# Kernel tuning notes

Measured on AMD Instinct MI355X. Metric: run time of the kernel, lower is better.

Reference implementation:

```python
import jax, jax.numpy as jnp
import numpy as np

B, L, D, H = 2, 2048, 1024, 16
NUM_BUCKETS, MAX_DISTANCE = 32, 128


def _rel_pos_buckets(qlen, klen, num_buckets, max_distance):
    """T5-style bidirectional relative position bucketing. Returns [qlen, klen] int32."""
    ctx = jnp.arange(qlen, dtype=jnp.int32)[:, None]
    mem = jnp.arange(klen, dtype=jnp.int32)[None, :]
    rel = mem - ctx  # memory_position - context_position
    nb = num_buckets // 2
    buckets = (rel > 0).astype(jnp.int32) * nb
    n = jnp.abs(rel)
    max_exact = nb // 2
    is_small = n < max_exact
    nf = jnp.maximum(n.astype(jnp.float32), 1.0)
    large = max_exact + (
        jnp.log(nf / max_exact) / np.float32(np.log(max_distance / max_exact)) * (nb - max_exact)
    ).astype(jnp.int32)
    large = jnp.minimum(large, nb - 1)
    return buckets + jnp.where(is_small, n, large)


def setup_inputs() -> dict:
    key = jax.random.key(0)
    ks = jax.random.split(key, 11)
    s = 0.02
    return {
        "x": jax.random.normal(ks[0], (B, L, D), dtype=jnp.float32),
        "mask": jax.random.randint(ks[1], (B, 1, L, L), 0, 2, dtype=jnp.int32),
        "Wq_w": jax.random.normal(ks[2], (D, D), dtype=jnp.float32) * s,
        "Wq_b": jnp.zeros((D,), dtype=jnp.float32),
        "Wk_w": jax.random.normal(ks[3], (D, D), dtype=jnp.float32) * s,
        "Wk_b": jnp.zeros((D,), dtype=jnp.float32),
        "Wv_w": jax.random.normal(ks[4], (D, D), dtype=jnp.float32) * s,
        "Wv_b": jnp.zeros((D,), dtype=jnp.float32),
        "Wo_w": jax.random.normal(ks[5], (D, D), dtype=jnp.float32) * s,
        "Wo_b": jnp.zeros((D,), dtype=jnp.float32),
        "rel_emb": jax.random.normal(ks[6], (NUM_BUCKETS, H), dtype=jnp.float32) * s,
    }


def reference(x, mask, Wq_w, Wq_b, Wk_w, Wk_b, Wv_w, Wv_b, Wo_w, Wo_b, rel_emb):
    b, l, d = x.shape
    h = H
    dk = d // h
    # torch Linear: y = x @ W.T + b
    Q = (x @ Wq_w.T + Wq_b).reshape(b, l, h, dk)
    K = (x @ Wk_w.T + Wk_b).reshape(b, l, h, dk)
    V = (x @ Wv_w.T + Wv_b).reshape(b, l, h, dk)
    scores = jnp.einsum("bqhd,bkhd->bhqk", Q, K) / jnp.sqrt(jnp.float32(dk))
    buckets = _rel_pos_buckets(l, l, NUM_BUCKETS, MAX_DISTANCE)  # [L, L]
    bias = rel_emb[buckets]  # [L, L, H]
    scores = scores + jnp.transpose(bias, (2, 0, 1))[None]  # [1, H, L, L]
    scores = jnp.where(mask == 0, jnp.float32(-1e9), scores)
    attn = jax.nn.softmax(scores, axis=-1)
    out = jnp.einsum("bhqk,bkhd->bqhd", attn, V).reshape(b, l, d)
    return out @ Wo_w.T + Wo_b
```

## Files before the change

### kernel.cpp

```cpp
#include <hip/hip_runtime.h>
#include <hip/hip_fp16.h>

#define B_ 2
#define L_ 2048
#define D_ 1024
#define H_ 16

typedef __attribute__((ext_vector_type(8))) _Float16 f16x8;
typedef __attribute__((ext_vector_type(4))) _Float16 f16x4;
typedef __attribute__((ext_vector_type(2))) __fp16 fp16x2;
typedef __attribute__((ext_vector_type(4))) float f32x4;

#define LOG2E 1.44269504088896f

__device__ __forceinline__ void gload_lds16(const void* g, void* l) {
  __builtin_amdgcn_global_load_lds(
      (const __attribute__((address_space(1))) unsigned int*)g,
      (__attribute__((address_space(3))) unsigned int*)l, 16, 0, 0);
}

__global__ __launch_bounds__(256) void cvt_all(
    const float* __restrict__ x, const float* __restrict__ Wq,
    const float* __restrict__ Wk, const float* __restrict__ Wv,
    const float* __restrict__ Wo, __half* __restrict__ xh,
    __half* __restrict__ wqh, __half* __restrict__ wkh,
    __half* __restrict__ wvh, __half* __restrict__ woh) {
  int i = blockIdx.x * 256 + threadIdx.x;
  const float* src;
  __half* dst;
  int j;
  if (i < 1048576) {
    src = x; dst = xh; j = i;
  } else {
    int k = i - 1048576;
    int wsel = k >> 18;
    j = k & 262143;
    src = wsel == 0 ? Wq : (wsel == 1 ? Wk : (wsel == 2 ? Wv : Wo));
    dst = wsel == 0 ? wqh : (wsel == 1 ? wkh : (wsel == 2 ? wvh : woh));
  }
  float4 v = ((const float4*)src)[j];
  __half2* o = (__half2*)(dst + (size_t)j * 4);
  o[0] = __floats2half2_rn(v.x, v.y);
  o[1] = __floats2half2_rn(v.z, v.w);
}

__global__ __launch_bounds__(256) void pack_mask(const int* __restrict__ m,
                                                 unsigned long long* __restrict__ bits) {
  int wword = blockIdx.x * 4 + (threadIdx.x >> 6);
  int lane = threadIdx.x & 63;
  int v = m[(size_t)wword * 64 + lane];
  unsigned long long bal = __ballot(v != 0);
  if (lane == 0) bits[wword] = bal;
}

__global__ __launch_bounds__(256) void bias_table(const float* __restrict__ rel_emb,
                                                  float* __restrict__ tab) {
  int i = blockIdx.x * 256 + threadIdx.x;
  if (i >= H_ * 4095) return;
  int h = i / 4095, idx = i - h * 4095;
  int rel = idx - 2047;
  int n = rel < 0 ? -rel : rel;
  int bkt;
  if (n < 8) {
    bkt = n;
  } else {
    float t = logf((float)n / 8.0f) / 2.772588722239781f * 8.0f;
    int v = 8 + (int)t;
    bkt = v < 15 ? v : 15;
  }
  if (rel > 0) bkt += 16;
  tab[i] = rel_emb[bkt * H_ + h] * LOG2E;
}

template <bool CT>
__device__ __forceinline__ void gemm_tile(const __half* __restrict__ A,
                                          const __half* __restrict__ Bw,
                                          int m0, int n0,
                                          __half* sA, __half* sB,
                                          f32x4 (&acc)[4][4],
                                          int lane, int wm, int wn, int t) {
  for (int k0 = 0; k0 < 1024; k0 += 64) {
    __syncthreads();
#pragma unroll
    for (int it = 0; it < 4; ++it) {
      int c = t + it * 256;
      int row = c >> 3, seg = c & 7;
      gload_lds16(A + ((size_t)(m0 + row) << 10) + k0 + seg * 8, sA + c * 8);
      gload_lds16(Bw + ((size_t)(n0 + row) << 10) + k0 + seg * 8, sB + c * 8);
    }
    __syncthreads();
#pragma unroll
    for (int kk = 0; kk < 2; ++kk) {
      const int off = kk * 32 + (lane >> 4) * 8;
      const int rr = lane & 15;
      f16x8 af[4], bf[4];
#pragma unroll
      for (int i = 0; i < 4; ++i) af[i] = *(const f16x8*)&sA[(wm * 64 + i * 16 + rr) * 64 + off];
#pragma unroll
      for (int i = 0; i < 4; ++i) bf[i] = *(const f16x8*)&sB[(wn * 64 + i * 16 + rr) * 64 + off];
#pragma unroll
      for (int mi = 0; mi < 4; ++mi)
#pragma unroll
        for (int ni = 0; ni < 4; ++ni) {
          if (CT)
            acc[mi][ni] = __builtin_amdgcn_mfma_f32_16x16x32_f16(bf[ni], af[mi], acc[mi][ni], 0, 0, 0);
          else
            acc[mi][ni] = __builtin_amdgcn_mfma_f32_16x16x32_f16(af[mi], bf[ni], acc[mi][ni], 0, 0, 0);
        }
    }
  }
}

__global__ __launch_bounds__(256) void gemm_qkv(
    const __half* __restrict__ xh,
    const __half* __restrict__ Wq, const __half* __restrict__ Wk, const __half* __restrict__ Wv,
    const float* __restrict__ bq, const float* __restrict__ bk, const float* __restrict__ bvv,
    __half* __restrict__ Qh, __half* __restrict__ Kh, __half* __restrict__ Vt) {
  __shared__ __align__(16) __half sA[128 * 64];
  __shared__ __align__(16) __half sB[128 * 64];
  const int lin = blockIdx.x;
  const int xcd = lin & 7, idx = lin >> 3;
  const int m0 = (xcd * 4 + (idx & 3)) * 128;
  const int ng = (idx >> 2) * 128;
  const int widx = ng >> 10;
  const int n0 = ng & 1023;
  const __half* Bw = widx == 0 ? Wq : (widx == 1 ? Wk : Wv);
  const float* bias = widx == 0 ? bq : (widx == 1 ? bk : bvv);
  const int t = threadIdx.x, lane = t & 63, w = t >> 6;
  const int wm = w >> 1, wn = w & 1;
  const int lg = lane >> 4, lr = lane & 15;
  f32x4 acc[4][4] = {};
  if (widx == 2) {
    gemm_tile<false>(xh, Bw, m0, n0, sA, sB, acc, lane, wm, wn, t);
#pragma unroll
    for (int mi = 0; mi < 4; ++mi)
#pragma unroll
      for (int ni = 0; ni < 4; ++ni) {
        int m = m0 + wm * 64 + mi * 16 + lg * 4;
        int n = n0 + wn * 64 + ni * 16 + lr;
        float bvx = bias[n];
        int b = m >> 11, l = m & 2047, hh = n >> 6, dd = n & 63;
        f32x4 a = acc[mi][ni];
        size_t base = ((size_t)((b * 16 + hh) * 64 + dd)) * 2048 + l;
        __half2 p0 = __floats2half2_rn(a.x + bvx, a.y + bvx);
        __half2 p1 = __floats2half2_rn(a.z + bvx, a.w + bvx);
        *(__half2*)(Vt + base) = p0;
        *(__half2*)(Vt + base + 2) = p1;
      }
  } else {
    gemm_tile<true>(xh, Bw, m0, n0, sA, sB, acc, lane, wm, wn, t);
    __half* dst = widx == 0 ? Qh : Kh;
    const float scf = widx == 0 ? 0.125f * LOG2E : 1.0f;
#pragma unroll
    for (int mi = 0; mi < 4; ++mi)
#pragma unroll
      for (int ni = 0; ni < 4; ++ni) {
        int m = m0 + wm * 64 + mi * 16 + lr;
        int n = n0 + wn * 64 + ni * 16 + 4 * lg;
        f32x4 bb = *(const f32x4*)&bias[n];
        int b = m >> 11, l = m & 2047, hh = n >> 6, dd = n & 63;
        f16x4 ov;
#pragma unroll
        for (int r = 0; r < 4; ++r) ov[r] = (_Float16)((acc[mi][ni][r] + bb[r]) * scf);
        *(f16x4*)(dst + (((size_t)(b * 16 + hh)) * 2048 + l) * 64 + dd) = ov;
      }
  }
}

__global__ __launch_bounds__(256) void gemm_out(
    const __half* __restrict__ AO, const __half* __restrict__ Wo,
    const float* __restrict__ bo, float* __restrict__ out) {
  __shared__ __align__(16) __half sA[128 * 64];
  __shared__ __align__(16) __half sB[128 * 64];
  const int lin = blockIdx.x;
  const int xcd = lin & 7, idx = lin >> 3;
  const int m0 = (xcd * 4 + (idx & 3)) * 128;
  const int n0 = (idx >> 2) * 128;
  const int t = threadIdx.x, lane = t & 63, w = t >> 6;
  const int wm = w >> 1, wn = w & 1;
  const int lg = lane >> 4, lr = lane & 15;
  f32x4 acc[4][4] = {};
  gemm_tile<true>(AO, Wo, m0, n0, sA, sB, acc, lane, wm, wn, t);
#pragma unroll
  for (int mi = 0; mi < 4; ++mi)
#pragma unroll
    for (int ni = 0; ni < 4; ++ni) {
      int m = m0 + wm * 64 + mi * 16 + lr;
      int n = n0 + wn * 64 + ni * 16 + 4 * lg;
      f32x4 bb = *(const f32x4*)&bo[n];
      f32x4 vv;
#pragma unroll
      for (int r = 0; r < 4; ++r) vv[r] = acc[mi][ni][r] + bb[r];
      *(f32x4*)(out + (size_t)m * 1024 + n) = vv;
    }
}

__device__ __forceinline__ void stage_kv(const __half* __restrict__ Kb,
                                         const __half* __restrict__ Vb, int kt,
                                         __half* kdst, __half* vdst, int t) {
#pragma unroll
  for (int it = 0; it < 2; ++it) {
    int c = t + it * 256;
    int row = c >> 3, seg = c & 7;
    int gs = (seg ^ row) & 7;
    gload_lds16(Kb + ((size_t)(kt + row) << 6) + gs * 8, kdst + c * 8);
    gload_lds16(Vb + ((size_t)row << 11) + kt + gs * 8, vdst + c * 8);
  }
}

__device__ __forceinline__ void attn_tile(
    const __half* kb, const __half* vb,
    unsigned long long mwv, int diff,
    f16x8 aq0, f16x8 aq1,
    const float* sbias, const __half2* lutm2,
    float c_neg, float c_pos, int lg, int lr,
    f32x4 (&o)[4], f32x4& osum, f16x4 ones) {
  __builtin_amdgcn_s_setprio(1);
  f32x4 s[4] = {};
#pragma unroll
  for (int ct = 0; ct < 4; ++ct) {
    int row = ct * 16 + lr;
    const __half* rb = &kb[row * 64];
    f16x8 kf0 = *(const f16x8*)(rb + ((8 * lg) ^ ((row & 7) << 3)));
    f16x8 kf1 = *(const f16x8*)(rb + ((32 + 8 * lg) ^ ((row & 7) << 3)));
    s[ct] = __builtin_amdgcn_mfma_f32_16x16x32_f16(kf0, aq0, s[ct], 0, 0, 0);
    s[ct] = __builtin_amdgcn_mfma_f32_16x16x32_f16(kf1, aq1, s[ct], 0, 0, 0);
  }
  __builtin_amdgcn_s_setprio(0);

  f16x4 bvA[4], bvB[4];
#pragma unroll
  for (int dt = 0; dt < 4; ++dt) {
    int row = dt * 16 + lr;
    bvA[dt] = *(const f16x4*)&vb[row * 64 + ((4 * lg) ^ ((row & 7) << 3))];
  }

  float tsc = 1.0f;
  if (diff >= 143) {
    tsc = exp2f(c_pos);
  } else if (diff <= -191) {
    tsc = exp2f(c_neg);
  } else {
    const int ibase = diff + 4 * lg - lr + 128;
#pragma unroll
    for (int ct = 0; ct < 4; ++ct)
#pragma unroll
      for (int r = 0; r < 4; ++r) {
        int idx = ibase + 16 * ct + r;
        idx = idx < 0 ? 0 : (idx > 256 ? 256 : idx);
        s[ct][r] += sbias[idx];
      }
  }
  const __half th = __float2half(tsc);
  const __half2 ts2{th, th};

  f16x4 pa[4];
#pragma unroll
  for (int ct = 0; ct < 4; ++ct) {
    unsigned bits = (unsigned)(mwv >> (16 * ct + 4 * lg)) & 15u;
    __half2 m01 = __hmul2(lutm2[bits * 2], ts2), m23 = __hmul2(lutm2[bits * 2 + 1], ts2);
    fp16x2 p01 = __builtin_amdgcn_cvt_pkrtz(exp2f(s[ct][0]), exp2f(s[ct][1]));
    fp16x2 p23 = __builtin_amdgcn_cvt_pkrtz(exp2f(s[ct][2]), exp2f(s[ct][3]));
    f16x4 pc;
    ((__half2*)&pc)[0] = __hmul2(*(__half2*)&p01, m01);
    ((__half2*)&pc)[1] = __hmul2(*(__half2*)&p23, m23);
    pa[ct] = pc;
  }

  __builtin_amdgcn_s_setprio(1);
#pragma unroll
  for (int dt = 0; dt < 4; ++dt) {
    int row = dt * 16 + lr;
    bvB[dt] = *(const f16x4*)&vb[row * 64 + ((16 + 4 * lg) ^ ((row & 7) << 3))];
  }
  osum = __builtin_amdgcn_mfma_f32_16x16x16f16(ones, pa[0], osum, 0, 0, 0);
#pragma unroll
  for (int dt = 0; dt < 4; ++dt)
    o[dt] = __builtin_amdgcn_mfma_f32_16x16x16f16(bvA[dt], pa[0], o[dt], 0, 0, 0);

#pragma unroll
  for (int dt = 0; dt < 4; ++dt) {
    int row = dt * 16 + lr;
    bvA[dt] = *(const f16x4*)&vb[row * 64 + ((32 + 4 * lg) ^ ((row & 7) << 3))];
  }
  osum = __builtin_amdgcn_mfma_f32_16x16x16f16(ones, pa[1], osum, 0, 0, 0);
#pragma unroll
  for (int dt = 0; dt < 4; ++dt)
    o[dt] = __builtin_amdgcn_mfma_f32_16x16x16f16(bvB[dt], pa[1], o[dt], 0, 0, 0);

#pragma unroll
  for (int dt = 0; dt < 4; ++dt) {
    int row = dt * 16 + lr;
    bvB[dt] = *(const f16x4*)&vb[row * 64 + ((48 + 4 * lg) ^ ((row & 7) << 3))];
  }
  osum = __builtin_amdgcn_mfma_f32_16x16x16f16(ones, pa[2], osum, 0, 0, 0);
#pragma unroll
  for (int dt = 0; dt < 4; ++dt)
    o[dt] = __builtin_amdgcn_mfma_f32_16x16x16f16(bvA[dt], pa[2], o[dt], 0, 0, 0);

  osum = __builtin_amdgcn_mfma_f32_16x16x16f16(ones, pa[3], osum, 0, 0, 0);
#pragma unroll
  for (int dt = 0; dt < 4; ++dt)
    o[dt] = __builtin_amdgcn_mfma_f32_16x16x16f16(bvB[dt], pa[3], o[dt], 0, 0, 0);
  __builtin_amdgcn_s_setprio(0);
}

__global__ __launch_bounds__(256, 4) void attn(
    const __half* __restrict__ Qh, const __half* __restrict__ Kh,
    const __half* __restrict__ Vt, const unsigned long long* __restrict__ mb64,
    const float* __restrict__ tab, __half* __restrict__ AO) {
  const int id = blockIdx.x;
  const int ii = id >> 3;
  const int bh = (id & 7) * 4 + (ii >> 5);
  const int q0 = (ii & 31) * 64;
  const int b = bh >> 4, h = bh & 15;
  const int t = threadIdx.x, lane = t & 63, w = t >> 6;
  const int lg = lane >> 4, lr = lane & 15;

  __shared__ __align__(16) __half sK[2][64 * 64];
  __shared__ __align__(16) __half sV[2][64 * 64];
  __shared__ float sbias[260];
  __shared__ __align__(8) __half lutm[16][4];

  for (int i = t; i < 257; i += 256) sbias[i] = tab[h * 4095 + 1919 + i];
  if (t < 64) {
    int e = t >> 2, j = t & 3;
    lutm[e][j] = ((e >> j) & 1) ? __half(1.0f) : __half(0.0f);
  }

  const size_t bh2048 = (size_t)bh * 2048;
  const int qrow = q0 + w * 16 + lr;
  const __half* qp = Qh + (bh2048 + qrow) * 64 + lg * 8;
  f16x8 aq0 = *(const f16x8*)qp;
  f16x8 aq1 = *(const f16x8*)(qp + 32);

  const __half* Kb = Kh + bh2048 * 64;
  const __half* Vb = Vt + bh2048 * 64;
  const unsigned long long* mrow = mb64 + ((size_t)(b * 2048 + qrow)) * 32;

  f32x4 o[4] = {};
  f32x4 osum = {};
  const f16x4 ones = {(_Float16)1.f, (_Float16)1.f, (_Float16)1.f, (_Float16)1.f};
  const __half2* lutm2 = (const __half2*)&lutm[0][0];

  unsigned long long mw0 = mrow[0], mw1 = mrow[1];

  stage_kv(Kb, Vb, 0, sK[0], sV[0], t);
  __syncthreads();
  const float c_neg = sbias[0], c_pos = sbias[256];
  const int dbase = -q0 - w * 16;

  for (int k0 = 0; k0 < L_; k0 += 128) {
    stage_kv(Kb, Vb, k0 + 64, sK[1], sV[1], t);
    unsigned long long mwa = mrow[(k0 >> 6) + 2];
    attn_tile(sK[0], sV[0], mw0, k0 + dbase, aq0, aq1, sbias, lutm2,
              c_neg, c_pos, lg, lr, o, osum, ones);
    __syncthreads();

    if (k0 + 128 < L_) stage_kv(Kb, Vb, k0 + 128, sK[0], sV[0], t);
    unsigned long long mwb = mrow[(k0 >> 6) + 3];
    attn_tile(sK[1], sV[1], mw1, k0 + 64 + dbase, aq0, aq1, sbias, lutm2,
              c_neg, c_pos, lg, lr, o, osum, ones);
    __syncthreads();

    mw0 = mwa;
    mw1 = mwb;
  }
  const float rl = 1.0f / osum[0];
  const size_t qbase = ((size_t)(b * L_ + q0 + w * 16 + lr)) * D_ + h * 64;
#pragma unroll
  for (int dt = 0; dt < 4; ++dt) {
    f16x4 ov;
#pragma unroll
    for (int r = 0; r < 4; ++r) ov[r] = (_Float16)(o[dt][r] * rl);
    *(f16x4*)(AO + qbase + dt * 16 + 4 * lg) = ov;
  }
}

extern "C" void kernel_launch(void* const* d_in, const int* in_sizes, int n_in,
                              void* d_out, int out_size, void* d_ws, size_t ws_size,
                              hipStream_t stream) {
  const float* x = (const float*)d_in[0];
  const int* mask = (const int*)d_in[1];
  const float* Wq_w = (const float*)d_in[2];
  const float* Wq_b = (const float*)d_in[3];
  const float* Wk_w = (const float*)d_in[4];
  const float* Wk_b = (const float*)d_in[5];
  const float* Wv_w = (const float*)d_in[6];
  const float* Wv_b = (const float*)d_in[7];
  const float* Wo_w = (const float*)d_in[8];
  const float* Wo_b = (const float*)d_in[9];
  const float* rel_emb = (const float*)d_in[10];
  float* out = (float*)d_out;

  char* ws = (char*)d_ws;
  const size_t MB = 1024 * 1024;
  __half* xh = (__half*)(ws);
  __half* wqh = (__half*)(ws + 8 * MB);
  __half* wkh = (__half*)(ws + 10 * MB);
  __half* wvh = (__half*)(ws + 12 * MB);
  __half* woh = (__half*)(ws + 14 * MB);
  __half* Qh = (__half*)(ws + 16 * MB);
  __half* Kh = (__half*)(ws + 24 * MB);
  __half* Vt = (__half*)(ws + 32 * MB);
  unsigned long long* mb64 = (unsigned long long*)(ws + 40 * MB);
  float* tab = (float*)(ws + 48 * MB);
  __half* AO = xh;

  cvt_all<<<8192, 256, 0, stream>>>(x, Wq_w, Wk_w, Wv_w, Wo_w, xh, wqh, wkh, wvh, woh);
  pack_mask<<<32768, 256, 0, stream>>>(mask, mb64);
  bias_table<<<256, 256, 0, stream>>>(rel_emb, tab);

  gemm_qkv<<<768, 256, 0, stream>>>(xh, wqh, wkh, wvh, Wq_b, Wk_b, Wv_b, Qh, Kh, Vt);
  attn<<<1024, 256, 0, stream>>>(Qh, Kh, Vt, mb64, tab, AO);
  gemm_out<<<256, 256, 0, stream>>>(AO, woh, Wo_b, out);
}
```

Baseline: 178.9 us.

## Merge prep kernels into one launch, shrink output GEMM tiles, pin attn occupancy

Folds the fp16 conversion, mask bit-packing and bias-table kernels into a single launch that branches on block index, removing two kernel launches and their gaps. The output projection GEMM moves from 128x128 tiles on 256 blocks to 64x64 tiles on 1024 blocks so more CUs are busy, at the cost of less data reuse per tile and more global traffic. The attention kernel's occupancy hint changes from a launch_bounds minimum to an explicit waves_per_eu(4,4) attribute.

```diff
diff --git a/kernel.cpp b/kernel.cpp
--- a/kernel.cpp
+++ b/kernel.cpp
@@ -19,57 +19,56 @@
       (__attribute__((address_space(3))) unsigned int*)l, 16, 0, 0);
 }
 
-__global__ __launch_bounds__(256) void cvt_all(
+__global__ __launch_bounds__(256) void prep(
     const float* __restrict__ x, const float* __restrict__ Wq,
     const float* __restrict__ Wk, const float* __restrict__ Wv,
-    const float* __restrict__ Wo, __half* __restrict__ xh,
-    __half* __restrict__ wqh, __half* __restrict__ wkh,
-    __half* __restrict__ wvh, __half* __restrict__ woh) {
-  int i = blockIdx.x * 256 + threadIdx.x;
-  const float* src;
-  __half* dst;
-  int j;
-  if (i < 1048576) {
-    src = x; dst = xh; j = i;
+    const float* __restrict__ Wo, const int* __restrict__ m,
+    const float* __restrict__ rel_emb,
+    __half* __restrict__ xh, __half* __restrict__ wqh, __half* __restrict__ wkh,
+    __half* __restrict__ wvh, __half* __restrict__ woh,
+    unsigned long long* __restrict__ bits, float* __restrict__ tab) {
+  const int bid = blockIdx.x;
+  if (bid < 8192) {
+    int i = bid * 256 + threadIdx.x;
+    const float* src;
+    __half* dst;
+    int j;
+    if (i < 1048576) {
+      src = x; dst = xh; j = i;
+    } else {
+      int k = i - 1048576;
+      int wsel = k >> 18;
+      j = k & 262143;
+      src = wsel == 0 ? Wq : (wsel == 1 ? Wk : (wsel == 2 ? Wv : Wo));
+      dst = wsel == 0 ? wqh : (wsel == 1 ? wkh : (wsel == 2 ? wvh : woh));
+    }
+    float4 v = ((const float4*)src)[j];
+    __half2* o = (__half2*)(dst + (size_t)j * 4);
+    o[0] = __floats2half2_rn(v.x, v.y);
+    o[1] = __floats2half2_rn(v.z, v.w);
+  } else if (bid < 40960) {
+    int wword = (bid - 8192) * 4 + (threadIdx.x >> 6);
+    int lane = threadIdx.x & 63;
+    int v = m[(size_t)wword * 64 + lane];
+    unsigned long long bal = __ballot(v != 0);
+    if (lane == 0) bits[wword] = bal;
   } else {
-    int k = i - 1048576;
-    int wsel = k >> 18;
-    j = k & 262143;
-    src = wsel == 0 ? Wq : (wsel == 1 ? Wk : (wsel == 2 ? Wv : Wo));
-    dst = wsel == 0 ? wqh : (wsel == 1 ? wkh : (wsel == 2 ? wvh : woh));
-  }
-  float4 v = ((const float4*)src)[j];
-  __half2* o = (__half2*)(dst + (size_t)j * 4);
-  o[0] = __floats2half2_rn(v.x, v.y);
-  o[1] = __floats2half2_rn(v.z, v.w);
-}
-
-__global__ __launch_bounds__(256) void pack_mask(const int* __restrict__ m,
-                                                 unsigned long long* __restrict__ bits) {
-  int wword = blockIdx.x * 4 + (threadIdx.x >> 6);
-  int lane = threadIdx.x & 63;
-  int v = m[(size_t)wword * 64 + lane];
-  unsigned long long bal = __ballot(v != 0);
-  if (lane == 0) bits[wword] = bal;
-}
-
-__global__ __launch_bounds__(256) void bias_table(const float* __restrict__ rel_emb,
-                                                  float* __restrict__ tab) {
-  int i = blockIdx.x * 256 + threadIdx.x;
-  if (i >= H_ * 4095) return;
-  int h = i / 4095, idx = i - h * 4095;
-  int rel = idx - 2047;
-  int n = rel < 0 ? -rel : rel;
-  int bkt;
-  if (n < 8) {
-    bkt = n;
-  } else {
-    float t = logf((float)n / 8.0f) / 2.772588722239781f * 8.0f;
-    int v = 8 + (int)t;
-    bkt = v < 15 ? v : 15;
-  }
-  if (rel > 0) bkt += 16;
-  tab[i] = rel_emb[bkt * H_ + h] * LOG2E;
+    int i = (bid - 40960) * 256 + threadIdx.x;
+    if (i >= H_ * 4095) return;
+    int h = i / 4095, idx = i - h * 4095;
+    int rel = idx - 2047;
+    int n = rel < 0 ? -rel : rel;
+    int bkt;
+    if (n < 8) {
+      bkt = n;
+    } else {
+      float t = logf((float)n / 8.0f) / 2.772588722239781f * 8.0f;
+      int v = 8 + (int)t;
+      bkt = v < 15 ? v : 15;
+    }
+    if (rel > 0) bkt += 16;
+    tab[i] = rel_emb[bkt * H_ + h] * LOG2E;
+  }
 }
 
 template <bool CT>
@@ -170,28 +169,52 @@
 __global__ __launch_bounds__(256) void gemm_out(
     const __half* __restrict__ AO, const __half* __restrict__ Wo,
     const float* __restrict__ bo, float* __restrict__ out) {
-  __shared__ __align__(16) __half sA[128 * 64];
-  __shared__ __align__(16) __half sB[128 * 64];
+  __shared__ __align__(16) __half sA[64 * 64];
+  __shared__ __align__(16) __half sB[64 * 64];
   const int lin = blockIdx.x;
   const int xcd = lin & 7, idx = lin >> 3;
-  const int m0 = (xcd * 4 + (idx & 3)) * 128;
-  const int n0 = (idx >> 2) * 128;
+  const int m0 = (xcd * 8 + (idx & 7)) * 64;
+  const int n0 = (idx >> 3) * 64;
   const int t = threadIdx.x, lane = t & 63, w = t >> 6;
   const int wm = w >> 1, wn = w & 1;
   const int lg = lane >> 4, lr = lane & 15;
-  f32x4 acc[4][4] = {};
-  gemm_tile<true>(AO, Wo, m0, n0, sA, sB, acc, lane, wm, wn, t);
-#pragma unroll
-  for (int mi = 0; mi < 4; ++mi)
-#pragma unroll
-    for (int ni = 0; ni < 4; ++ni) {
-      int m = m0 + wm * 64 + mi * 16 + lr;
-      int n = n0 + wn * 64 + ni * 16 + 4 * lg;
-      f32x4 bb = *(const f32x4*)&bo[n];
+  f32x4 acc[2][2] = {};
+  for (int k0 = 0; k0 < 1024; k0 += 64) {
+    __syncthreads();
+#pragma unroll
+    for (int it = 0; it < 2; ++it) {
+      int c = t + it * 256;
+      int row = c >> 3, seg = c & 7;
+      gload_lds16(AO + ((size_t)(m0 + row) << 10) + k0 + seg * 8, sA + c * 8);
+      gload_lds16(Wo + ((size_t)(n0 + row) << 10) + k0 + seg * 8, sB + c * 8);
+    }
+    __syncthreads();
+#pragma unroll
+    for (int kk = 0; kk < 2; ++kk) {
+      const int off = kk * 32 + lg * 8;
+      f16x8 af[2], bf[2];
+#pragma unroll
+      for (int i = 0; i < 2; ++i) af[i] = *(const f16x8*)&sA[(wm * 32 + i * 16 + lr) * 64 + off];
+#pragma unroll
+      for (int i = 0; i < 2; ++i) bf[i] = *(const f16x8*)&sB[(wn * 32 + i * 16 + lr) * 64 + off];
+#pragma unroll
+      for (int mi = 0; mi < 2; ++mi)
+#pragma unroll
+        for (int ni = 0; ni < 2; ++ni)
+          acc[mi][ni] = __builtin_amdgcn_mfma_f32_16x16x32_f16(bf[ni], af[mi], acc[mi][ni], 0, 0, 0);
+    }
+  }
+#pragma unroll
+  for (int mi = 0; mi < 2; ++mi)
+#pragma unroll
+    for (int ni = 0; ni < 2; ++ni) {
+      int mm = m0 + wm * 32 + mi * 16 + lr;
+      int nn = n0 + wn * 32 + ni * 16 + 4 * lg;
+      f32x4 bb = *(const f32x4*)&bo[nn];
       f32x4 vv;
 #pragma unroll
       for (int r = 0; r < 4; ++r) vv[r] = acc[mi][ni][r] + bb[r];
-      *(f32x4*)(out + (size_t)m * 1024 + n) = vv;
+      *(f32x4*)(out + (size_t)mm * 1024 + nn) = vv;
     }
 }
 
@@ -305,7 +328,7 @@
   __builtin_amdgcn_s_setprio(0);
 }
 
-__global__ __launch_bounds__(256, 4) void attn(
+__global__ __attribute__((amdgpu_waves_per_eu(4, 4))) __launch_bounds__(256) void attn(
     const __half* __restrict__ Qh, const __half* __restrict__ Kh,
     const __half* __restrict__ Vt, const unsigned long long* __restrict__ mb64,
     const float* __restrict__ tab, __half* __restrict__ AO) {
@@ -407,11 +430,9 @@
   float* tab = (float*)(ws + 48 * MB);
   __half* AO = xh;
 
-  cvt_all<<<8192, 256, 0, stream>>>(x, Wq_w, Wk_w, Wv_w, Wo_w, xh, wqh, wkh, wvh, woh);
-  pack_mask<<<32768, 256, 0, stream>>>(mask, mb64);
-  bias_table<<<256, 256, 0, stream>>>(rel_emb, tab);
-
+  prep<<<41216, 256, 0, stream>>>(x, Wq_w, Wk_w, Wv_w, Wo_w, mask, rel_emb,
+                                  xh, wqh, wkh, wvh, woh, mb64, tab);
   gemm_qkv<<<768, 256, 0, stream>>>(xh, wqh, wkh, wvh, Wq_b, Wk_b, Wv_b, Qh, Kh, Vt);
   attn<<<1024, 256, 0, stream>>>(Qh, Kh, Vt, mb64, tab, AO);
-  gemm_out<<<256, 256, 0, stream>>>(AO, woh, Wo_b, out);
-}
+  gemm_out<<<1024, 256, 0, stream>>>(AO, woh, Wo_b, out);
+}
```

After: 170.6 us. -4.7%, faster.
